# Kernel optimization log

Measured on AMD Instinct MI355X. Metric: run time of the kernel, lower is better.

## Reference

```python
import jax, jax.numpy as jnp
import numpy as np

D = 512   # dense write dimension
M = 64    # number of experts
B = 16    # per-expert sparse code width
N = 8192  # tokens
K = 4     # experts per token (top-k)


def _normalize_U(U):
    # UnitColNormPadded(dim=1): each column of the (D+1, b) expert matrix
    # is rescaled to unit L2 norm along the padded (D+1) axis.
    nrm = jnp.sqrt(jnp.sum(U * U, axis=1, keepdims=True))
    return U / nrm


def setup_inputs() -> dict:
    key = jax.random.key(0)
    k1, k2, k3 = jax.random.split(key, 3)
    h_sparse = jax.random.normal(k1, (N, K, B), dtype=jnp.float32)
    topk_idxs = jax.random.randint(k2, (N, K), 0, M)
    U = jax.random.normal(k3, (M, D + 1, B), dtype=jnp.float32)
    return {"h_sparse": h_sparse, "topk_idxs": topk_idxs, "U": U}


def reference(h_sparse, topk_idxs, U):
    Un = _normalize_U(U)                      # (m, D+1, b)
    U_active = Un[topk_idxs][:, :, :D, :]     # gather -> (N, k, D, b)
    writes = jnp.einsum('nkdb,nkb->nd', U_active, h_sparse)   # (N, D)
    h_recon = jnp.einsum('nkdb,nd->nkb', U_active, writes)    # (N, k, b)
    h_target = jax.lax.stop_gradient(h_sparse)
    diff = h_recon - h_target
    writer_aux_loss = jnp.mean(diff * diff)
    return writes, writer_aux_loss
```

## Files before the change

### kernel.cpp

```cpp
#include <hip/hip_runtime.h>

#define DD 512
#define MM 64
#define BB 16
#define NN 8192
#define KK 4
#define DP1 513
#define CAP 1024
#define GPE 8
#define NPAIR (NN * KK)

#define CNT_B  0
#define BKT_B  256
#define INV_B  131328
#define U_B    135424
#define UT_B   1184000
#define WBF_B  2232576
#define PART_B 10621184
#define WS_NEED 44175616

typedef unsigned int uint;
typedef unsigned short ushort;
typedef __attribute__((ext_vector_type(8))) short short8;
typedef __attribute__((ext_vector_type(4))) float f32x4;

struct __align__(8) U16x4 { ushort x, y, z, w; };

__device__ __forceinline__ ushort f2bf(float f) {
    uint u = __builtin_bit_cast(uint, f);
    uint r = (u + 0x7FFFu + ((u >> 16) & 1u)) >> 16;
    return (ushort)r;
}
__device__ __forceinline__ float bf2f(ushort s) {
    return __builtin_bit_cast(float, (uint)s << 16);
}

__global__ __launch_bounds__(256) void norm_kernel(
    const float* __restrict__ U, float* __restrict__ inv_norm,
    float* __restrict__ loss_slot)
{
    const int m = blockIdx.x, t = threadIdx.x;
    const float* Um = U + (long)m * DP1 * BB;
    float acc = 0.f;
    for (int idx = t; idx < DP1 * BB; idx += 256) {
        float v = Um[idx];
        acc += v * v;
    }
    __shared__ float s[256];
    s[t] = acc;
    __syncthreads();
    if (t < BB) {
        float tot = 0.f;
        #pragma unroll
        for (int j = 0; j < 16; ++j) tot += s[t + 16 * j];
        inv_norm[m * BB + t] = rsqrtf(tot);
    }
    if (m == 0 && t == 0) *loss_slot = 0.f;
}

__global__ __launch_bounds__(256) void pack_kernel(
    const float* __restrict__ U, void* __restrict__ ws)
{
    const int m = blockIdx.x >> 2, sl = blockIdx.x & 3;
    const int t = threadIdx.x;
    const float* Um = U + (long)m * DP1 * BB + (long)sl * 128 * BB;
    const float* invp = (const float*)((const char*)ws + INV_B) + m * BB;
    ushort* ub = (ushort*)((char*)ws + U_B) + (long)m * DD * BB + sl * 128 * BB;
    ushort* ut = (ushort*)((char*)ws + UT_B) + (long)m * BB * DD + sl * 128;

    __shared__ float inv_s[BB];
    __shared__ ushort tr[BB][136];

    if (t < BB) inv_s[t] = invp[t];
    __syncthreads();

    #pragma unroll
    for (int iter = 0; iter < 4; ++iter) {
        const int i = t + iter * 256;
        const int e0 = 2 * i;
        const int dl = e0 >> 4, b0 = e0 & 15;
        const float2 v = *(const float2*)(Um + e0);
        const ushort bv0 = f2bf(v.x * inv_s[b0]);
        const ushort bv1 = f2bf(v.y * inv_s[b0 + 1]);
        *(uint*)(ub + e0) = (uint)bv0 | ((uint)bv1 << 16);
        tr[b0][dl] = bv0;
        tr[b0 + 1][dl] = bv1;
    }
    __syncthreads();

    {
        const int b = t >> 4, doff = (t & 15) * 8;
        const uint4 val = *(const uint4*)&tr[b][doff];
        *(uint4*)(ut + (long)b * DD + doff) = val;
    }
}

__global__ __launch_bounds__(256) void build_buckets(
    const int* __restrict__ topk, void* __restrict__ ws)
{
    int* cnt = (int*)ws;
    ushort* bkt = (ushort*)((char*)ws + BKT_B);
    __shared__ int lc[MM], lb[MM];
    const int t = threadIdx.x;
    if (t < MM) lc[t] = 0;
    __syncthreads();
    const int p = blockIdx.x * 256 + t;
    const int e = topk[p];
    const int my = atomicAdd(&lc[e], 1);
    __syncthreads();
    if (t < MM) lb[t] = atomicAdd(&cnt[t], lc[t]);
    __syncthreads();
    bkt[e * CAP + lb[e] + my] = (ushort)p;
}

__global__ __launch_bounds__(256) void pass_writes_mfma(
    const float* __restrict__ h_sparse, void* __restrict__ ws)
{
    const int e = blockIdx.x >> 3, g = blockIdx.x & 7;
    const int wave = threadIdx.x >> 6, lane = threadIdx.x & 63;
    const int quad = lane >> 4, l15 = lane & 15;

    const int* cnt = (const int*)ws;
    const ushort* bkt = (const ushort*)((const char*)ws + BKT_B);
    const ushort* Ue = (const ushort*)((const char*)ws + U_B) + (long)e * DD * BB;
    ushort* part = (ushort*)((char*)ws + PART_B);

    const int c  = cnt[e];
    const int lo = (c * g) >> 3;
    const int hi = (c * (g + 1)) >> 3;

    for (int base = lo + wave * 16; base < hi; base += 64) {
        const int pidx = base + l15;
        const bool valid = pidx < hi;
        const int id = valid ? (int)bkt[e * CAP + pidx] : 0;
        const int n = id >> 2, k = id & 3;

        short8 bfrag = (short8)0;
        if (quad < 2 && valid) {
            const float4* hp = (const float4*)(h_sparse + (long)id * BB + quad * 8);
            const float4 h0 = hp[0], h1 = hp[1];
            bfrag[0] = (short)f2bf(h0.x); bfrag[1] = (short)f2bf(h0.y);
            bfrag[2] = (short)f2bf(h0.z); bfrag[3] = (short)f2bf(h0.w);
            bfrag[4] = (short)f2bf(h1.x); bfrag[5] = (short)f2bf(h1.y);
            bfrag[6] = (short)f2bf(h1.z); bfrag[7] = (short)f2bf(h1.w);
        }
        ushort* prow = part + ((long)(k * NN + n) << 9);

        #pragma unroll 4
        for (int dt = 0; dt < 32; ++dt) {
            short8 afrag = (short8)0;
            if (quad < 2)
                afrag = *(const short8*)(Ue + ((long)(dt * 16 + l15) << 4) + quad * 8);
            f32x4 acc = {0.f, 0.f, 0.f, 0.f};
            acc = __builtin_amdgcn_mfma_f32_16x16x32_bf16(afrag, bfrag, acc, 0, 0, 0);
            if (valid) {
                U16x4 st;
                st.x = f2bf(acc[0]); st.y = f2bf(acc[1]);
                st.z = f2bf(acc[2]); st.w = f2bf(acc[3]);
                *(U16x4*)(prow + dt * 16 + quad * 4) = st;
            }
        }
    }
}

__global__ __launch_bounds__(256) void reduce_w(
    void* __restrict__ ws, float* __restrict__ out)
{
    const uint4* part4 = (const uint4*)((const char*)ws + PART_B);
    uint4* wbf4 = (uint4*)((char*)ws + WBF_B);
    const int gsz = NN * DD / 8;
    const int gid = blockIdx.x * 256 + threadIdx.x;

    const uint4 v0 = part4[gid];
    const uint4 v1 = part4[(long)gsz + gid];
    const uint4 v2 = part4[2L * gsz + gid];
    const uint4 v3 = part4[3L * gsz + gid];

    float s[8];
    s[0] = bf2f((ushort)v0.x) + bf2f((ushort)v1.x) + bf2f((ushort)v2.x) + bf2f((ushort)v3.x);
    s[1] = bf2f((ushort)(v0.x >> 16)) + bf2f((ushort)(v1.x >> 16)) + bf2f((ushort)(v2.x >> 16)) + bf2f((ushort)(v3.x >> 16));
    s[2] = bf2f((ushort)v0.y) + bf2f((ushort)v1.y) + bf2f((ushort)v2.y) + bf2f((ushort)v3.y);
    s[3] = bf2f((ushort)(v0.y >> 16)) + bf2f((ushort)(v1.y >> 16)) + bf2f((ushort)(v2.y >> 16)) + bf2f((ushort)(v3.y >> 16));
    s[4] = bf2f((ushort)v0.z) + bf2f((ushort)v1.z) + bf2f((ushort)v2.z) + bf2f((ushort)v3.z);
    s[5] = bf2f((ushort)(v0.z >> 16)) + bf2f((ushort)(v1.z >> 16)) + bf2f((ushort)(v2.z >> 16)) + bf2f((ushort)(v3.z >> 16));
    s[6] = bf2f((ushort)v0.w) + bf2f((ushort)v1.w) + bf2f((ushort)v2.w) + bf2f((ushort)v3.w);
    s[7] = bf2f((ushort)(v0.w >> 16)) + bf2f((ushort)(v1.w >> 16)) + bf2f((ushort)(v2.w >> 16)) + bf2f((ushort)(v3.w >> 16));

    float4* out4 = (float4*)out;
    out4[(long)gid * 2 + 0] = make_float4(s[0], s[1], s[2], s[3]);
    out4[(long)gid * 2 + 1] = make_float4(s[4], s[5], s[6], s[7]);

    uint4 pk;
    pk.x = (uint)f2bf(s[0]) | ((uint)f2bf(s[1]) << 16);
    pk.y = (uint)f2bf(s[2]) | ((uint)f2bf(s[3]) << 16);
    pk.z = (uint)f2bf(s[4]) | ((uint)f2bf(s[5]) << 16);
    pk.w = (uint)f2bf(s[6]) | ((uint)f2bf(s[7]) << 16);
    wbf4[gid] = pk;
}

__global__ __launch_bounds__(256) void pass_recon_mfma(
    const float* __restrict__ h_sparse, void* __restrict__ ws,
    float* __restrict__ out)
{
    const int e = blockIdx.x >> 3, g = blockIdx.x & 7;
    const int wave = threadIdx.x >> 6, lane = threadIdx.x & 63;
    const int quad = lane >> 4, l15 = lane & 15;
    const int t = threadIdx.x;

    const int* cnt = (const int*)ws;
    const ushort* bkt = (const ushort*)((const char*)ws + BKT_B);
    const ushort* Ute = (const ushort*)((const char*)ws + UT_B) + (long)e * BB * DD;
    const ushort* wbf = (const ushort*)((const char*)ws + WBF_B);

    __shared__ float loss_blk;
    if (t == 0) loss_blk = 0.f;
    __syncthreads();

    const int c  = cnt[e];
    const int lo = (c * g) >> 3;
    const int hi = (c * (g + 1)) >> 3;

    float lsum = 0.f;

    for (int base = lo + wave * 16; base < hi; base += 64) {
        const int pidx = base + l15;
        const bool valid = pidx < hi;
        const int id = valid ? (int)bkt[e * CAP + pidx] : 0;
        const int n = id >> 2;
        const ushort* wrow = wbf + ((long)n << 9);

        f32x4 acc = {0.f, 0.f, 0.f, 0.f};

        #pragma unroll 4
        for (int kk = 0; kk < 16; ++kk) {
            const int doff = kk * 32 + quad * 8;
            const short8 afrag = *(const short8*)(wrow + doff);
            const short8 bfrag = *(const short8*)(Ute + (long)l15 * DD + doff);
            acc = __builtin_amdgcn_mfma_f32_16x16x32_bf16(afrag, bfrag, acc, 0, 0, 0);
        }

        #pragma unroll
        for (int r = 0; r < 4; ++r) {
            const int pr = base + quad * 4 + r;
            if (pr < hi) {
                const int id2 = (int)bkt[e * CAP + pr];
                const float h = h_sparse[(long)id2 * BB + l15];
                const float d = acc[r] - h;
                lsum += d * d;
            }
        }
    }

    #pragma unroll
    for (int off = 32; off > 0; off >>= 1) lsum += __shfl_xor(lsum, off, 64);
    if (lane == 0 && lsum != 0.f) atomicAdd(&loss_blk, lsum);
    __syncthreads();
    if (t == 0 && loss_blk != 0.f)
        atomicAdd(out + (long)NN * DD, loss_blk * (1.0f / ((float)NN * KK * BB)));
}

__global__ __launch_bounds__(256) void dense_write_kernel(
    const float* __restrict__ h_sparse,
    const int*   __restrict__ topk,
    const float* __restrict__ U,
    const float* __restrict__ inv_norm,
    float* __restrict__ out)
{
    const int n = blockIdx.x;
    const int t = threadIdx.x;

    __shared__ float hs[KK * BB];
    __shared__ float ho[KK * BB];
    __shared__ float inv_s[KK * BB];
    __shared__ int   eidx[KK];
    __shared__ float w_s[DD];
    __shared__ float red[256];

    if (t < KK) eidx[t] = topk[n * KK + t];
    __syncthreads();
    if (t < KK * BB) {
        const int k = t / BB, b = t % BB;
        const float h  = h_sparse[(long)n * KK * BB + t];
        const float iv = inv_norm[eidx[k] * BB + b];
        ho[t]    = h;
        inv_s[t] = iv;
        hs[t]    = h * iv;
    }
    __syncthreads();

    #pragma unroll
    for (int dd = 0; dd < 2; ++dd) {
        const int d = t + dd * 256;
        float w = 0.f;
        #pragma unroll
        for (int k = 0; k < KK; ++k) {
            const float4* row = (const float4*)(U + ((long)eidx[k] * DP1 + d) * BB);
            #pragma unroll
            for (int q = 0; q < 4; ++q) {
                const float4 u4 = row[q];
                w += u4.x * hs[k * BB + 4 * q + 0];
                w += u4.y * hs[k * BB + 4 * q + 1];
                w += u4.z * hs[k * BB + 4 * q + 2];
                w += u4.w * hs[k * BB + 4 * q + 3];
            }
        }
        w_s[d] = w;
        out[(long)n * DD + d] = w;
    }
    __syncthreads();

    {
        const int pair = t & 63;
        const int k = pair >> 4, b = pair & 15;
        const int ch = t >> 6;
        const float* Ucol = U + (long)eidx[k] * DP1 * BB + b;
        float p = 0.f;
        #pragma unroll 8
        for (int d = ch * 128; d < ch * 128 + 128; ++d) {
            p += Ucol[(long)d * BB] * w_s[d];
        }
        red[t] = p;
    }
    __syncthreads();

    if (t < 64) {
        const float recon = (red[t] + red[t + 64] + red[t + 128] + red[t + 192]) * inv_s[t];
        const float diff  = recon - ho[t];
        float sq = diff * diff;
        #pragma unroll
        for (int off = 32; off > 0; off >>= 1) sq += __shfl_down(sq, off, 64);
        if (t == 0) {
            atomicAdd(out + (long)NN * DD, sq * (1.0f / ((float)NN * KK * BB)));
        }
    }
}


extern "C" void kernel_launch(void* const* d_in, const int* in_sizes, int n_in,
                              void* d_out, int out_size, void* d_ws, size_t ws_size,
                              hipStream_t stream) {
    const float* h_sparse = (const float*)d_in[0];
    const int*   topk     = (const int*)d_in[1];
    const float* U        = (const float*)d_in[2];
    float* out = (float*)d_out;

    if (ws_size >= (size_t)WS_NEED) {
        hipMemsetAsync(d_ws, 0, 256, stream);
        hipLaunchKernelGGL(norm_kernel, dim3(MM), dim3(256), 0, stream,
                           U, (float*)((char*)d_ws + INV_B), out + (long)NN * DD);
        hipLaunchKernelGGL(pack_kernel, dim3(MM * 4), dim3(256), 0, stream,
                           U, d_ws);
        hipLaunchKernelGGL(build_buckets, dim3(NPAIR / 256), dim3(256), 0, stream,
                           topk, d_ws);
        hipLaunchKernelGGL(pass_writes_mfma, dim3(MM * GPE), dim3(256), 0, stream,
                           h_sparse, d_ws);
        hipLaunchKernelGGL(reduce_w, dim3(NN * DD / 8 / 256), dim3(256), 0, stream,
                           d_ws, out);
        hipLaunchKernelGGL(pass_recon_mfma, dim3(MM * GPE), dim3(256), 0, stream,
                           h_sparse, d_ws, out);
    } else {
        float* inv_norm = (float*)d_ws;
        hipLaunchKernelGGL(norm_kernel, dim3(MM), dim3(256), 0, stream,
                           U, inv_norm, out + (long)NN * DD);
        hipLaunchKernelGGL(dense_write_kernel, dim3(NN), dim3(256), 0, stream,
                           h_sparse, topk, U, inv_norm, out);
    }
}
```

Before: 136.7 us.

## Fuse norm and pack kernels; widen partial-write stores via lane shuffles

```diff
diff --git a/kernel.cpp b/kernel.cpp
--- a/kernel.cpp
+++ b/kernel.cpp
@@ -12,7 +12,6 @@
 
 #define CNT_B  0
 #define BKT_B  256
-#define INV_B  131328
 #define U_B    135424
 #define UT_B   1184000
 #define WBF_B  2232576
@@ -24,8 +23,6 @@
 typedef __attribute__((ext_vector_type(8))) short short8;
 typedef __attribute__((ext_vector_type(4))) float f32x4;
 
-struct __align__(8) U16x4 { ushort x, y, z, w; };
-
 __device__ __forceinline__ ushort f2bf(float f) {
     uint u = __builtin_bit_cast(uint, f);
     uint r = (u + 0x7FFFu + ((u >> 16) & 1u)) >> 16;
@@ -35,64 +32,60 @@
     return __builtin_bit_cast(float, (uint)s << 16);
 }
 
-__global__ __launch_bounds__(256) void norm_kernel(
-    const float* __restrict__ U, float* __restrict__ inv_norm,
+__global__ __launch_bounds__(256) void prep_kernel(
+    const float* __restrict__ U, void* __restrict__ ws,
     float* __restrict__ loss_slot)
 {
     const int m = blockIdx.x, t = threadIdx.x;
     const float* Um = U + (long)m * DP1 * BB;
-    float acc = 0.f;
-    for (int idx = t; idx < DP1 * BB; idx += 256) {
-        float v = Um[idx];
-        acc += v * v;
-    }
-    __shared__ float s[256];
-    s[t] = acc;
+
+    __shared__ float red[256];
+    __shared__ float inv_s[BB];
+    __shared__ ushort tr[BB][DD + 8];
+
+    float a = 0.f;
+    for (int i = t; i < DP1 * BB; i += 256) { float v = Um[i]; a += v * v; }
+    red[t] = a;
     __syncthreads();
     if (t < BB) {
         float tot = 0.f;
         #pragma unroll
-        for (int j = 0; j < 16; ++j) tot += s[t + 16 * j];
-        inv_norm[m * BB + t] = rsqrtf(tot);
-    }
-    if (m == 0 && t == 0) *loss_slot = 0.f;
-}
-
-__global__ __launch_bounds__(256) void pack_kernel(
-    const float* __restrict__ U, void* __restrict__ ws)
-{
-    const int m = blockIdx.x >> 2, sl = blockIdx.x & 3;
-    const int t = threadIdx.x;
-    const float* Um = U + (long)m * DP1 * BB + (long)sl * 128 * BB;
-    const float* invp = (const float*)((const char*)ws + INV_B) + m * BB;
-    ushort* ub = (ushort*)((char*)ws + U_B) + (long)m * DD * BB + sl * 128 * BB;
-    ushort* ut = (ushort*)((char*)ws + UT_B) + (long)m * BB * DD + sl * 128;
-
-    __shared__ float inv_s[BB];
-    __shared__ ushort tr[BB][136];
-
-    if (t < BB) inv_s[t] = invp[t];
-    __syncthreads();
+        for (int j = 0; j < 16; ++j) tot += red[t + 16 * j];
+        inv_s[t] = rsqrtf(tot);
+    }
+    __syncthreads();
+
+    ushort* ub = (ushort*)((char*)ws + U_B) + (long)m * DD * BB;
+    ushort* ut = (ushort*)((char*)ws + UT_B) + (long)m * BB * DD;
 
     #pragma unroll
-    for (int iter = 0; iter < 4; ++iter) {
+    for (int iter = 0; iter < 16; ++iter) {
         const int i = t + iter * 256;
         const int e0 = 2 * i;
-        const int dl = e0 >> 4, b0 = e0 & 15;
+        const int d = e0 >> 4, b0 = e0 & 15;
         const float2 v = *(const float2*)(Um + e0);
         const ushort bv0 = f2bf(v.x * inv_s[b0]);
         const ushort bv1 = f2bf(v.y * inv_s[b0 + 1]);
         *(uint*)(ub + e0) = (uint)bv0 | ((uint)bv1 << 16);
-        tr[b0][dl] = bv0;
-        tr[b0 + 1][dl] = bv1;
+        tr[b0][d] = bv0;
+        tr[b0 + 1][d] = bv1;
     }
     __syncthreads();
 
     {
-        const int b = t >> 4, doff = (t & 15) * 8;
-        const uint4 val = *(const uint4*)&tr[b][doff];
-        *(uint4*)(ut + (long)b * DD + doff) = val;
-    }
+        const int b = t >> 4, base = (t & 15) * 32;
+        #pragma unroll
+        for (int j = 0; j < 4; ++j) {
+            const int doff = base + j * 8;
+            uint4 val;
+            val.x = (uint)tr[b][doff + 0] | ((uint)tr[b][doff + 1] << 16);
+            val.y = (uint)tr[b][doff + 2] | ((uint)tr[b][doff + 3] << 16);
+            val.z = (uint)tr[b][doff + 4] | ((uint)tr[b][doff + 5] << 16);
+            val.w = (uint)tr[b][doff + 6] | ((uint)tr[b][doff + 7] << 16);
+            *(uint4*)(ut + (long)b * DD + doff) = val;
+        }
+    }
+    if (m == 0 && t == 0) *loss_slot = 0.f;
 }
 
 __global__ __launch_bounds__(256) void build_buckets(
@@ -146,18 +139,38 @@
         }
         ushort* prow = part + ((long)(k * NN + n) << 9);
 
-        #pragma unroll 4
-        for (int dt = 0; dt < 32; ++dt) {
-            short8 afrag = (short8)0;
-            if (quad < 2)
-                afrag = *(const short8*)(Ue + ((long)(dt * 16 + l15) << 4) + quad * 8);
-            f32x4 acc = {0.f, 0.f, 0.f, 0.f};
-            acc = __builtin_amdgcn_mfma_f32_16x16x32_bf16(afrag, bfrag, acc, 0, 0, 0);
+        #pragma unroll 2
+        for (int dt = 0; dt < 32; dt += 2) {
+            short8 a0 = (short8)0, a1 = (short8)0;
+            if (quad < 2) {
+                a0 = *(const short8*)(Ue + ((long)(dt * 16 + l15) << 4) + quad * 8);
+                a1 = *(const short8*)(Ue + ((long)((dt + 1) * 16 + l15) << 4) + quad * 8);
+            }
+            f32x4 z = {0.f, 0.f, 0.f, 0.f};
+            f32x4 c0 = __builtin_amdgcn_mfma_f32_16x16x32_bf16(a0, bfrag, z, 0, 0, 0);
+            f32x4 c1 = __builtin_amdgcn_mfma_f32_16x16x32_bf16(a1, bfrag, z, 0, 0, 0);
+
+            uint p0x = (uint)f2bf(c0[0]) | ((uint)f2bf(c0[1]) << 16);
+            uint p0y = (uint)f2bf(c0[2]) | ((uint)f2bf(c0[3]) << 16);
+            uint p1x = (uint)f2bf(c1[0]) | ((uint)f2bf(c1[1]) << 16);
+            uint p1y = (uint)f2bf(c1[2]) | ((uint)f2bf(c1[3]) << 16);
+            uint q0x = __shfl_xor((int)p0x, 16, 64);
+            uint q0y = __shfl_xor((int)p0y, 16, 64);
+            uint q1x = __shfl_xor((int)p1x, 16, 64);
+            uint q1y = __shfl_xor((int)p1y, 16, 64);
+
             if (valid) {
-                U16x4 st;
-                st.x = f2bf(acc[0]); st.y = f2bf(acc[1]);
-                st.z = f2bf(acc[2]); st.w = f2bf(acc[3]);
-                *(U16x4*)(prow + dt * 16 + quad * 4) = st;
+                uint4 st;
+                int sdt;
+                if ((quad & 1) == 0) {
+                    st.x = p0x; st.y = p0y; st.z = q0x; st.w = q0y;
+                    sdt = dt;
+                } else {
+                    st.x = q1x; st.y = q1y; st.z = p1x; st.w = p1y;
+                    sdt = dt + 1;
+                }
+                const int srow = (quad & 2) ? 8 : 0;
+                *(uint4*)(prow + sdt * 16 + srow) = st;
             }
         }
     }
@@ -257,6 +270,30 @@
     __syncthreads();
     if (t == 0 && loss_blk != 0.f)
         atomicAdd(out + (long)NN * DD, loss_blk * (1.0f / ((float)NN * KK * BB)));
+}
+
+__global__ __launch_bounds__(256) void norm_kernel(
+    const float* __restrict__ U, float* __restrict__ inv_norm,
+    float* __restrict__ loss_slot)
+{
+    const int m = blockIdx.x;
+    const int t = threadIdx.x;
+    const float* Um = U + (long)m * DP1 * BB;
+    float acc = 0.f;
+    for (int idx = t; idx < DP1 * BB; idx += 256) {
+        float v = Um[idx];
+        acc += v * v;
+    }
+    __shared__ float s[256];
+    s[t] = acc;
+    __syncthreads();
+    if (t < BB) {
+        float tot = 0.f;
+        #pragma unroll
+        for (int j = 0; j < 16; ++j) tot += s[t + 16 * j];
+        inv_norm[m * BB + t] = rsqrtf(tot);
+    }
+    if (m == 0 && t == 0) *loss_slot = 0.f;
 }
 
 __global__ __launch_bounds__(256) void dense_write_kernel(
@@ -346,10 +383,8 @@
 
     if (ws_size >= (size_t)WS_NEED) {
         hipMemsetAsync(d_ws, 0, 256, stream);
-        hipLaunchKernelGGL(norm_kernel, dim3(MM), dim3(256), 0, stream,
-                           U, (float*)((char*)d_ws + INV_B), out + (long)NN * DD);
-        hipLaunchKernelGGL(pack_kernel, dim3(MM * 4), dim3(256), 0, stream,
-                           U, d_ws);
+        hipLaunchKernelGGL(prep_kernel, dim3(MM), dim3(256), 0, stream,
+                           U, d_ws, out + (long)NN * DD);
         hipLaunchKernelGGL(build_buckets, dim3(NPAIR / 256), dim3(256), 0, stream,
                            topk, d_ws);
         hipLaunchKernelGGL(pass_writes_mfma, dim3(MM * GPE), dim3(256), 0, stream,
```

Measured after the change: 127.2 us. -6.9%, faster.
